# Optimization experiments

Hardware: AMD Instinct MI355X
Metric: run time of the kernel (lower is better)

The kernel has to match this reference:

```python
import jax, jax.numpy as jnp
import numpy as np

KS = 2            # kernel_size
NUM_SHARED = 3    # len(num_shared_channels)
NBR_PARAM = 3     # nbr_param_layers
COUT = 128        # num_shared_channels[-1] == num_inputs
NUM_INPUTS = 128
D_R = 320         # ts2vec_output_dims
GEN_LEN = NBR_PARAM * COUT * COUT * KS


def _causal_conv(x, w, b, d):
    # x: [N, Ci, T], w: [Co, Ci, K], b: [Co]; left-pad (K-1)*d == pad+chomp in torch
    N, Ci, T = x.shape
    K = w.shape[-1]
    pad = (K - 1) * d
    xp = jnp.pad(x, ((0, 0), (0, 0), (pad, 0)))
    out = jnp.zeros((N, w.shape[0], T), dtype=x.dtype)
    for k in range(K):  # K==2, tiny static loop
        out = out + jnp.einsum('oc,nct->not', w[:, :, k], xp[:, :, k * d:k * d + T])
    return out + b[None, :, None]


def _causal_conv_group(x, w, d):
    # groups=N conv with per-sample weights. x: [N, C, T], w: [N, Co, C, K], no bias
    N, C, T = x.shape
    K = w.shape[-1]
    pad = (K - 1) * d
    xp = jnp.pad(x, ((0, 0), (0, 0), (pad, 0)))
    out = jnp.zeros((N, w.shape[1], T), dtype=x.dtype)
    for k in range(K):
        out = out + jnp.einsum('noc,nct->not', w[..., k], xp[:, :, k * d:k * d + T])
    return out


def setup_inputs() -> dict:
    key = jax.random.key(0)
    ks = jax.random.split(key, 12)
    N, T = 16, 1024
    x = jax.random.normal(ks[0], (N, T, NUM_INPUTS), dtype=jnp.float32)
    r = jax.random.normal(ks[1], (N, D_R), dtype=jnp.float32)
    # shared TemporalBlock params (in==out==COUT, so no downsample conv)
    wscale = 1.0 / np.sqrt(COUT * KS)
    shared_w1 = wscale * jax.random.normal(ks[2], (NUM_SHARED, COUT, COUT, KS), dtype=jnp.float32)
    shared_b1 = 0.01 * jax.random.normal(ks[3], (NUM_SHARED, COUT), dtype=jnp.float32)
    shared_w2 = wscale * jax.random.normal(ks[4], (NUM_SHARED, COUT, COUT, KS), dtype=jnp.float32)
    shared_b2 = 0.01 * jax.random.normal(ks[5], (NUM_SHARED, COUT), dtype=jnp.float32)
    # hypernetwork (f_param_generator) + additive base weights (last_conv_layers)
    fparam_W = 0.01 * jax.random.normal(ks[6], (GEN_LEN, D_R), dtype=jnp.float32)
    fparam_b = 0.01 * jax.random.normal(ks[7], (GEN_LEN,), dtype=jnp.float32)
    last_bias = 0.001 * jax.random.normal(ks[8], (GEN_LEN,), dtype=jnp.float32) + 1.0 / (KS * COUT)
    # output head
    lin_W = (1.0 / np.sqrt(COUT)) * jax.random.normal(ks[9], (NUM_INPUTS, COUT), dtype=jnp.float32)
    lin_b = 0.01 * jax.random.normal(ks[10], (NUM_INPUTS,), dtype=jnp.float32)
    return {"x": x, "r": r, "f_out_same_in_size": 1,
            "shared_w1": shared_w1, "shared_b1": shared_b1,
            "shared_w2": shared_w2, "shared_b2": shared_b2,
            "fparam_W": fparam_W, "fparam_b": fparam_b, "last_bias": last_bias,
            "lin_W": lin_W, "lin_b": lin_b}


def reference(x, r, f_out_same_in_size, shared_w1, shared_b1, shared_w2, shared_b2,
              fparam_W, fparam_b, last_bias, lin_W, lin_b):
    N, T, _ = x.shape
    h = jnp.swapaxes(x, 1, 2)  # [N, C, T]
    # shared TemporalBlocks (dropout p=0 -> identity)
    for i in range(NUM_SHARED):
        d = 2 ** i
        res = h
        a = jax.nn.relu(_causal_conv(h, shared_w1[i], shared_b1[i], d))
        a = jax.nn.relu(_causal_conv(a, shared_w2[i], shared_b2[i], d))
        h = jax.nn.relu(a + res)
    # hypernet-generated per-sample grouped conv layers
    gen = r @ fparam_W.T + fparam_b + last_bias           # [N, GEN_LEN]
    allw = gen.reshape(NBR_PARAM, N, COUT, COUT, KS)      # same layout as torch .view
    for i in range(NBR_PARAM):
        d = 2 ** (NUM_SHARED + i)
        res = h
        c = _causal_conv_group(h, allw[i], d)
        h = jax.nn.relu(jax.nn.relu(c) + res)             # relu(dropout(relu(c)) + res), p=0
    out = jnp.einsum('nct,oc->nto', h, lin_W) + lin_b     # [N, T, NUM_INPUTS]
    if not f_out_same_in_size:
        out = out[:, -1, :]
    return out
```

## Files before the change

### kernel.cpp

```cpp
#include <hip/hip_runtime.h>

#define NB    16
#define TLEN  1024
#define CCH   128
#define DR    320

typedef _Float16 h8 __attribute__((ext_vector_type(8)));
typedef _Float16 h4 __attribute__((ext_vector_type(4)));
typedef _Float16 h2 __attribute__((ext_vector_type(2)));
typedef float    f4 __attribute__((ext_vector_type(4)));

__device__ __forceinline__ void gload16h(const _Float16* g, _Float16* l) {
  __builtin_amdgcn_global_load_lds(
      (const __attribute__((address_space(1))) void*)g,
      (__attribute__((address_space(3))) void*)l, 16, 0, 0);
}
__device__ __forceinline__ void gload16f(const float* g, float* l) {
  __builtin_amdgcn_global_load_lds(
      (const __attribute__((address_space(1))) void*)g,
      (__attribute__((address_space(3))) void*)l, 16, 0, 0);
}

__global__ __launch_bounds__(256) void k_init(const float* __restrict__ x,
                                              const float* __restrict__ w1,
                                              const float* __restrict__ w2,
                                              const float* __restrict__ linw,
                                              const float* __restrict__ fb,
                                              const float* __restrict__ lb,
                                              _Float16* __restrict__ h0,
                                              _Float16* __restrict__ Wsh,
                                              _Float16* __restrict__ linWh,
                                              float* __restrict__ fblb2) {
  int i = blockIdx.x * 256 + threadIdx.x;
  const float4* src = (const float4*)x + (size_t)i * 2;
  float4 a = src[0], b = src[1];
  h8 v;
  v[0] = (_Float16)a.x; v[1] = (_Float16)a.y; v[2] = (_Float16)a.z; v[3] = (_Float16)a.w;
  v[4] = (_Float16)b.x; v[5] = (_Float16)b.y; v[6] = (_Float16)b.z; v[7] = (_Float16)b.w;
  *(h8*)(h0 + (size_t)i * 8) = v;

  if (i < 6 * 32768) {
    int c = i & 127, k = (i >> 7) & 1, o = (i >> 8) & 127, i3 = i >> 15;
    const float* srcw = (i3 < 3) ? (w1 + i3 * 32768) : (w2 + (i3 - 3) * 32768);
    Wsh[i] = (_Float16)srcw[(o * 128 + c) * 2 + k];
  }
  if (i < 16384) linWh[i] = (_Float16)linw[i];
  if (i < 98304) fblb2[i] = fb[i] + lb[i];
}

struct SGen {
  float buf[3][32 * DR];
  float csc[4][16][16];
  float fbl[512];
};
struct SPair {
  _Float16 hin[84 * 128];
  _Float16 a[80 * 128];
};
union alignas(16) SU { SGen g; SPair p; };

__device__ __forceinline__ void gen_body(SGen& S, int bid, int tid,
                                         const float* __restrict__ r,
                                         const float* __restrict__ fW,
                                         const float* __restrict__ fblb2,
                                         _Float16* __restrict__ wg) {
  constexpr int NT = 16;
  const size_t rbase = (size_t)bid * 512;

  const int l = tid & 63, w = tid >> 6;
  const int l15 = l & 15, lh = l >> 4;
  const int rt = w >> 1, kh = w & 1;

  f4 rx[5], ry[5];
  const float* rp = r + l15 * DR + kh * 160 + lh * 8;
#pragma unroll
  for (int cb = 0; cb < 5; cb++) {
    rx[cb] = *(const f4*)(rp + cb * 32);
    ry[cb] = *(const f4*)(rp + cb * 32 + 4);
  }
  if (tid < 128) gload16f(fblb2 + rbase + tid * 4, S.fbl + tid * 4);
#pragma unroll
  for (int t = 0; t < 3; t++) {
    const float* s = fW + (rbase + (size_t)t * 32) * DR;
#pragma unroll
    for (int i = 0; i < 10; i++) {
      int f = tid + i * 256;
      gload16f(s + (size_t)f * 4, (float*)S.buf[t] + (size_t)f * 4);
    }
  }
  h8 bfr[5];
#pragma unroll
  for (int cb = 0; cb < 5; cb++) {
    h8 v;
    v[0] = (_Float16)rx[cb][0]; v[1] = (_Float16)rx[cb][1];
    v[2] = (_Float16)rx[cb][2]; v[3] = (_Float16)rx[cb][3];
    v[4] = (_Float16)ry[cb][0]; v[5] = (_Float16)ry[cb][1];
    v[6] = (_Float16)ry[cb][2]; v[7] = (_Float16)ry[cb][3];
    bfr[cb] = v;
  }
  asm volatile("s_waitcnt vmcnt(20) lgkmcnt(0)" ::: "memory");
  __builtin_amdgcn_s_barrier();
  __builtin_amdgcn_sched_barrier(0);

  const int rn = tid >> 4, rk = (tid >> 3) & 1, rcq = tid & 7;

  for (int j = 0; j < NT; j++) {
    const float* bp = (const float*)S.buf[j % 3];
    f4 acc = {0.f, 0.f, 0.f, 0.f};
    const float* arow = bp + (rt * 16 + l15) * DR + kh * 160 + lh * 8;
#pragma unroll
    for (int cb = 0; cb < 5; cb++) {
      f4 x = *(const f4*)(arow + cb * 32);
      f4 y = *(const f4*)(arow + cb * 32 + 4);
      h8 a;
      a[0] = (_Float16)x[0]; a[1] = (_Float16)x[1];
      a[2] = (_Float16)x[2]; a[3] = (_Float16)x[3];
      a[4] = (_Float16)y[0]; a[5] = (_Float16)y[1];
      a[6] = (_Float16)y[2]; a[7] = (_Float16)y[3];
      acc = __builtin_amdgcn_mfma_f32_16x16x32_f16(a, bfr[cb], acc, 0, 0, 0);
    }
#pragma unroll
    for (int rr = 0; rr < 4; rr++) S.csc[w][lh * 4 + rr][l15] = acc[rr];

    asm volatile("s_waitcnt lgkmcnt(0)" ::: "memory");
    __builtin_amdgcn_s_barrier();
    __builtin_amdgcn_sched_barrier(0);

    {
      const unsigned g32 = (unsigned)(rbase + (size_t)j * 32);
      const unsigned G = g32 >> 15, o = (g32 >> 8) & 127u, c0 = (g32 & 255u) >> 1;
      h2 v2;
#pragma unroll
      for (int i = 0; i < 2; i++) {
        int rl32 = (rcq * 2 + i) * 2 + rk;
        int hp = (rl32 >> 4) * 2, rr2 = rl32 & 15;
        float s = S.csc[hp][rr2][rn] + S.csc[hp + 1][rr2][rn] + S.fbl[j * 32 + rl32];
        v2[i] = (_Float16)s;
      }
      unsigned q = 3u * (unsigned)rn + G;
      *(h2*)&wg[(((size_t)q * 128 + o) * 2 + rk) * 128 + c0 + rcq * 2] = v2;
    }
    __builtin_amdgcn_sched_barrier(0);

    if (j + 3 < NT) {
      float* dstb = (float*)S.buf[j % 3];
      const float* src = fW + (rbase + (size_t)(j + 3) * 32) * DR;
#pragma unroll
      for (int i = 0; i < 10; i++) {
        int f = tid + i * 256;
        gload16f(src + (size_t)f * 4, dstb + (size_t)f * 4);
      }
    }

    if (j + 4 <= NT)
      asm volatile("s_waitcnt vmcnt(22) lgkmcnt(0)" ::: "memory");
    else if (j + 3 == NT)
      asm volatile("s_waitcnt vmcnt(12) lgkmcnt(0)" ::: "memory");
    else
      asm volatile("s_waitcnt vmcnt(0) lgkmcnt(0)" ::: "memory");
    __builtin_amdgcn_s_barrier();
    __builtin_amdgcn_sched_barrier(0);
  }
}

template <int D>
__device__ __forceinline__ void pair_body(SPair& S, int tx, int n, int tid,
                                          const _Float16* in, _Float16* out,
                                          const _Float16* w1p, const _Float16* w2p,
                                          const float* b1p, const float* b2p) {
  constexpr int HA = 16;
  constexpr int HI = HA + D;
  constexpr int RIN = 80 + D;
  static_assert(RIN * 128 <= sizeof(SPair::hin) / sizeof(_Float16), "hin size");
  _Float16* hin_l = S.hin;
  _Float16* a_l = S.a;
  const int t0 = tx * 64;
  const _Float16* inN = in + (size_t)n * (TLEN * CCH);

  if (tx == 0) {
    for (int f = tid; f < HI * 16; f += 256)
      *(int4*)(hin_l + (size_t)f * 8) = make_int4(0, 0, 0, 0);
    for (int f = HI * 16 + tid; f < RIN * 16; f += 256) {
      int p = f >> 4, l16 = f & 15;
      int c8 = (l16 ^ (p & 15)) << 3;
      gload16h(inN + (t0 - HI + p) * 128 + c8, hin_l + f * 8);
    }
  } else {
    for (int f = tid; f < RIN * 16; f += 256) {
      int p = f >> 4, l16 = f & 15;
      int c8 = (l16 ^ (p & 15)) << 3;
      gload16h(inN + (t0 - HI + p) * 128 + c8, hin_l + f * 8);
    }
  }
  __syncthreads();

  const int l = tid & 63, w = tid >> 6;
  const int l15 = l & 15, lh = l >> 4;
  const int o0 = w * 32;

  f4 acc1[2][5] = {};
#pragma unroll
  for (int tap = 0; tap < 2; tap++) {
#pragma unroll
    for (int cb = 0; cb < 4; cb++) {
      const int c0 = cb * 32 + lh * 8;
      h8 a[2], bfr[5];
#pragma unroll
      for (int i2 = 0; i2 < 2; i2++) {
        int o = o0 + i2 * 16 + l15;
        a[i2] = *(const h8*)&w1p[(o * 2 + tap) * 128 + c0];
      }
#pragma unroll
      for (int jt = 0; jt < 5; jt++) {
        int p = jt * 16 + l15 + tap * D;
        int cs = c0 ^ ((p & 15) << 3);
        bfr[jt] = *(const h8*)&hin_l[p * 128 + cs];
      }
#pragma unroll
      for (int i2 = 0; i2 < 2; i2++)
#pragma unroll
        for (int jt = 0; jt < 5; jt++)
          acc1[i2][jt] = __builtin_amdgcn_mfma_f32_16x16x32_f16(
              a[i2], bfr[jt], acc1[i2][jt], 0, 0, 0);
    }
  }
#pragma unroll
  for (int i2 = 0; i2 < 2; i2++) {
    f4 bv = *(const f4*)&b1p[o0 + i2 * 16 + lh * 4];
    const int base8 = o0 + i2 * 16 + (lh >> 1) * 8;
    const int sub = (lh & 1) * 4;
#pragma unroll
    for (int jt = 0; jt < 5; jt++) {
      int p = jt * 16 + l15;
      h4 sv;
      if (tx == 0 && jt == 0) {
        sv[0] = sv[1] = sv[2] = sv[3] = (_Float16)0.f;
      } else {
        f4 v = acc1[i2][jt];
#pragma unroll
        for (int rr = 0; rr < 4; rr++) sv[rr] = (_Float16)fmaxf(v[rr] + bv[rr], 0.f);
      }
      *(h4*)&a_l[p * 128 + (base8 ^ ((p & 15) << 3)) + sub] = sv;
    }
  }
  __syncthreads();

  f4 acc2[2][4] = {};
#pragma unroll
  for (int tap = 0; tap < 2; tap++) {
#pragma unroll
    for (int cb = 0; cb < 4; cb++) {
      const int c0 = cb * 32 + lh * 8;
      h8 a[2], bfr[4];
#pragma unroll
      for (int i2 = 0; i2 < 2; i2++) {
        int o = o0 + i2 * 16 + l15;
        a[i2] = *(const h8*)&w2p[(o * 2 + tap) * 128 + c0];
      }
#pragma unroll
      for (int jt = 0; jt < 4; jt++) {
        int pa = jt * 16 + l15 + (HA - D) + tap * D;
        int cs = c0 ^ ((pa & 15) << 3);
        bfr[jt] = *(const h8*)&a_l[pa * 128 + cs];
      }
#pragma unroll
      for (int i2 = 0; i2 < 2; i2++)
#pragma unroll
        for (int jt = 0; jt < 4; jt++)
          acc2[i2][jt] = __builtin_amdgcn_mfma_f32_16x16x32_f16(
              a[i2], bfr[jt], acc2[i2][jt], 0, 0, 0);
    }
  }

  _Float16* outN = out + (size_t)n * (TLEN * CCH);
#pragma unroll
  for (int i2 = 0; i2 < 2; i2++) {
    f4 bv = *(const f4*)&b2p[o0 + i2 * 16 + lh * 4];
    const int base8 = o0 + i2 * 16 + (lh >> 1) * 8;
    const int sub = (lh & 1) * 4;
#pragma unroll
    for (int jt = 0; jt < 4; jt++) {
      int t = t0 + jt * 16 + l15;
      int pr = jt * 16 + l15 + HA + D;
      h4 rv = *(const h4*)&hin_l[pr * 128 + (base8 ^ ((pr & 15) << 3)) + sub];
      f4 v = acc2[i2][jt];
      h4 sv;
#pragma unroll
      for (int rr = 0; rr < 4; rr++) {
        float z = fmaxf(v[rr] + bv[rr], 0.f);
        sv[rr] = (_Float16)fmaxf(z + (float)rv[rr], 0.f);
      }
      *(h4*)&outN[t * 128 + o0 + i2 * 16 + lh * 4] = sv;
    }
  }
}

__global__ __launch_bounds__(256, 1) void k_genpair(
    const float* __restrict__ r, const float* __restrict__ fW,
    const float* __restrict__ fblb2, _Float16* __restrict__ wg,
    const _Float16* __restrict__ h0, _Float16* __restrict__ h1,
    const _Float16* __restrict__ Wsh,
    const float* __restrict__ b1, const float* __restrict__ b2) {
  __shared__ SU su;
  const int bid = blockIdx.x, tid = threadIdx.x;
  if (bid < 192) {
    gen_body(su.g, bid, tid, r, fW, fblb2, wg);
  } else {
    int q = bid - 192;
    pair_body<1>(su.p, q & 15, q >> 4, tid, h0, h1,
                 Wsh, Wsh + 3 * 32768, b1, b2);
  }
}

template <int D, int NJ, bool GOUT>
__device__ __forceinline__ void pstage(const _Float16* __restrict__ w1p,
                                       const _Float16* __restrict__ w2p,
                                       const float* __restrict__ b1p,
                                       const float* __restrict__ b2p,
                                       const _Float16* __restrict__ inb,
                                       _Float16* __restrict__ ab,
                                       _Float16* __restrict__ outb,
                                       _Float16* __restrict__ goutN, int t0,
                                       int zlimA, int zlimO, int tid) {
  constexpr int NA = NJ + 1;
  const int l = tid & 63, w = tid >> 6;
  const int l15 = l & 15, lh = l >> 4;
  const int o0 = w * 32;
  const int base8 = o0 + (lh >> 1) * 8;
  const int sub = (lh & 1) * 4;

  f4 acc1[2][NA] = {};
#pragma unroll
  for (int tap = 0; tap < 2; tap++) {
#pragma unroll
    for (int cb = 0; cb < 4; cb++) {
      const int c0 = cb * 32 + lh * 8;
      h8 a[2], bfr[NA];
#pragma unroll
      for (int i2 = 0; i2 < 2; i2++) {
        int o = o0 + i2 * 16 + l15;
        a[i2] = *(const h8*)&w1p[(o * 2 + tap) * 128 + c0];
      }
#pragma unroll
      for (int jt = 0; jt < NA; jt++) {
        int p = jt * 16 + l15 + tap * D;
        int cs = c0 ^ ((p & 15) << 3);
        bfr[jt] = *(const h8*)&inb[p * 128 + cs];
      }
#pragma unroll
      for (int i2 = 0; i2 < 2; i2++)
#pragma unroll
        for (int jt = 0; jt < NA; jt++)
          acc1[i2][jt] = __builtin_amdgcn_mfma_f32_16x16x32_f16(
              a[i2], bfr[jt], acc1[i2][jt], 0, 0, 0);
    }
  }
#pragma unroll
  for (int i2 = 0; i2 < 2; i2++) {
    f4 bv = *(const f4*)&b1p[o0 + i2 * 16 + lh * 4];
    const int b8 = base8 + i2 * 16;
#pragma unroll
    for (int jt = 0; jt < NA; jt++) {
      int q = jt * 16 + l15;
      h4 sv;
      if (q < zlimA) {
        sv[0] = sv[1] = sv[2] = sv[3] = (_Float16)0.f;
      } else {
        f4 v = acc1[i2][jt];
#pragma unroll
        for (int rr = 0; rr < 4; rr++) sv[rr] = (_Float16)fmaxf(v[rr] + bv[rr], 0.f);
      }
      *(h4*)&ab[q * 128 + (b8 ^ ((q & 15) << 3)) + sub] = sv;
    }
  }
  __syncthreads();

  f4 acc2[2][NJ] = {};
#pragma unroll
  for (int tap = 0; tap < 2; tap++) {
#pragma unroll
    for (int cb = 0; cb < 4; cb++) {
      const int c0 = cb * 32 + lh * 8;
      h8 a[2], bfr[NJ];
#pragma unroll
      for (int i2 = 0; i2 < 2; i2++) {
        int o = o0 + i2 * 16 + l15;
        a[i2] = *(const h8*)&w2p[(o * 2 + tap) * 128 + c0];
      }
#pragma unroll
      for (int jt = 0; jt < NJ; jt++) {
        int pa = jt * 16 + l15 + (16 - 2 * D) + tap * D;
        int cs = c0 ^ ((pa & 15) << 3);
        bfr[jt] = *(const h8*)&ab[pa * 128 + cs];
      }
#pragma unroll
      for (int i2 = 0; i2 < 2; i2++)
#pragma unroll
        for (int jt = 0; jt < NJ; jt++)
          acc2[i2][jt] = __builtin_amdgcn_mfma_f32_16x16x32_f16(
              a[i2], bfr[jt], acc2[i2][jt], 0, 0, 0);
    }
  }
#pragma unroll
  for (int i2 = 0; i2 < 2; i2++) {
    f4 bv = *(const f4*)&b2p[o0 + i2 * 16 + lh * 4];
    const int b8 = base8 + i2 * 16;
#pragma unroll
    for (int jt = 0; jt < NJ; jt++) {
      int r = jt * 16 + l15;
      int pr = r + 16;
      h4 sv;
      if (r < zlimO) {
        sv[0] = sv[1] = sv[2] = sv[3] = (_Float16)0.f;
      } else {
        h4 rv = *(const h4*)&inb[pr * 128 + (b8 ^ ((pr & 15) << 3)) + sub];
        f4 v = acc2[i2][jt];
#pragma unroll
        for (int rr = 0; rr < 4; rr++) {
          float z = fmaxf(v[rr] + bv[rr], 0.f);
          sv[rr] = (_Float16)fmaxf(z + (float)rv[rr], 0.f);
        }
      }
      if (GOUT) {
        int t = t0 + r;
        *(h4*)&goutN[t * 128 + o0 + i2 * 16 + lh * 4] = sv;
      } else {
        *(h4*)&outb[r * 128 + (b8 ^ (l15 << 3)) + sub] = sv;
      }
    }
  }
}

__global__ __launch_bounds__(256) void k_pair24(const _Float16* __restrict__ in,
                                                _Float16* __restrict__ out,
                                                const _Float16* __restrict__ Wsh,
                                                const float* __restrict__ b1,
                                                const float* __restrict__ b2) {
  __shared__ _Float16 B0[104 * 128];
  __shared__ _Float16 B1[96 * 128];
  __shared__ _Float16 B2[88 * 128];
  const int tid = threadIdx.x;
  const int tx = blockIdx.x, n = blockIdx.y;
  const int t0 = tx * 64;
  const _Float16* inN = in + (size_t)n * (TLEN * CCH);

  for (int f = 96 * 16 + tid; f < 104 * 16; f += 256)
    *(int4*)(B0 + (size_t)f * 8) = make_int4(0, 0, 0, 0);
  for (int f = 80 * 16 + tid; f < 88 * 16; f += 256)
    *(int4*)(B2 + (size_t)f * 8) = make_int4(0, 0, 0, 0);

  if (tx == 0) {
    for (int f = tid; f < 32 * 16; f += 256)
      *(int4*)(B0 + (size_t)f * 8) = make_int4(0, 0, 0, 0);
    for (int f = 32 * 16 + tid; f < 96 * 16; f += 256) {
      int p = f >> 4, l16 = f & 15;
      int c8 = (l16 ^ (p & 15)) << 3;
      gload16h(inN + (t0 - 32 + p) * 128 + c8, B0 + f * 8);
    }
  } else {
    for (int f = tid; f < 96 * 16; f += 256) {
      int p = f >> 4, l16 = f & 15;
      int c8 = (l16 ^ (p & 15)) << 3;
      gload16h(inN + (t0 - 32 + p) * 128 + c8, B0 + f * 8);
    }
  }
  __syncthreads();

  pstage<2, 5, false>(Wsh + 1 * 32768, Wsh + 4 * 32768, b1 + 128, b2 + 128,
                      B0, B1, B2, nullptr, t0,
                      (tx == 0) ? 30 : 0, (tx == 0) ? 16 : 0, tid);
  __syncthreads();
  pstage<4, 4, true>(Wsh + 2 * 32768, Wsh + 5 * 32768, b1 + 256, b2 + 256,
                     B2, B1, nullptr,
                     out + (size_t)n * (TLEN * CCH), t0,
                     (tx == 0) ? 12 : 0, 0, tid);
}

template <int D, int NJ>
__device__ __forceinline__ void gstage(const _Float16* __restrict__ Wl,
                                       const _Float16* __restrict__ inb,
                                       _Float16* __restrict__ outb,
                                       int zlim, int tid) {
  const int l = tid & 63, w = tid >> 6;
  const int l15 = l & 15, lh = l >> 4;
  const int o0 = w * 32;
  f4 acc[2][NJ] = {};

#pragma unroll
  for (int tap = 0; tap < 2; tap++) {
#pragma unroll
    for (int cb = 0; cb < 4; cb++) {
      const int c0 = cb * 32 + 8 * lh;
      h8 a[2], bfr[NJ];
#pragma unroll
      for (int i2 = 0; i2 < 2; i2++) {
        int o = o0 + i2 * 16 + l15;
        int cs = c0 ^ ((o & 15) << 3);
        a[i2] = *(const h8*)&Wl[(o * 2 + tap) * 128 + cs];
      }
#pragma unroll
      for (int jt = 0; jt < NJ; jt++) {
        int p = jt * 16 + l15 + tap * D;
        int cs = c0 ^ ((p & 15) << 3);
        bfr[jt] = *(const h8*)&inb[p * 128 + cs];
      }
#pragma unroll
      for (int i2 = 0; i2 < 2; i2++)
#pragma unroll
        for (int jt = 0; jt < NJ; jt++)
          acc[i2][jt] = __builtin_amdgcn_mfma_f32_16x16x32_f16(
              a[i2], bfr[jt], acc[i2][jt], 0, 0, 0);
    }
  }

#pragma unroll
  for (int i2 = 0; i2 < 2; i2++) {
    const int base8 = o0 + i2 * 16 + (lh >> 1) * 8;
    const int sub = (lh & 1) * 4;
#pragma unroll
    for (int jt = 0; jt < NJ; jt++) {
      int rrow = jt * 16 + l15;
      int pr = rrow + D;
      h4 sv;
      if (rrow < zlim) {
        sv[0] = sv[1] = sv[2] = sv[3] = (_Float16)0.f;
      } else {
        h4 rv = *(const h4*)&inb[pr * 128 + (base8 ^ ((pr & 15) << 3)) + sub];
        f4 v = acc[i2][jt];
#pragma unroll
        for (int rr = 0; rr < 4; rr++) {
          float z = fmaxf(v[rr], 0.f);
          sv[rr] = (_Float16)fmaxf(z + (float)rv[rr], 0.f);
        }
      }
      *(h4*)&outb[rrow * 128 + (base8 ^ (l15 << 3)) + sub] = sv;
    }
  }
}

__global__ __launch_bounds__(256, 1) void k_group(const _Float16* __restrict__ in,
                                                  float* __restrict__ outp,
                                                  const _Float16* __restrict__ wg,
                                                  const _Float16* __restrict__ linWh,
                                                  const float* __restrict__ lbias) {
  __shared__ _Float16 bufA[120 * 128];
  __shared__ _Float16 bufB[112 * 128];
  __shared__ _Float16 Wl[256 * 128];
  const int tid = threadIdx.x;
  const int bid = blockIdx.x;
  const int n = (bid & 7) | (((bid >> 3) & 1) << 3);
  const int tx = bid >> 4;
  const int t0 = tx * 64;
  const _Float16* inN = in + (size_t)n * (TLEN * CCH);
  const _Float16* wp1 = wg + (size_t)n * 32768;
  const _Float16* wp2 = wg + 524288 + (size_t)n * 32768;
  const _Float16* wp3 = wg + 1048576 + (size_t)n * 32768;

  if (tx == 0) {
    for (int f = tid; f < 56 * 16; f += 256)
      *(int4*)(bufA + (size_t)f * 8) = make_int4(0, 0, 0, 0);
    for (int f = 56 * 16 + tid; f < 120 * 16; f += 256) {
      int p = f >> 4, l16 = f & 15;
      int c8 = (l16 ^ (p & 15)) << 3;
      gload16h(inN + (t0 - 56 + p) * 128 + c8, bufA + f * 8);
    }
  } else {
    for (int f = tid; f < 120 * 16; f += 256) {
      int p = f >> 4, l16 = f & 15;
      int c8 = (l16 ^ (p & 15)) << 3;
      gload16h(inN + (t0 - 56 + p) * 128 + c8, bufA + f * 8);
    }
  }
  for (int f = tid; f < 4096; f += 256) {
    int row = f >> 4, l16 = f & 15;
    int c8 = (l16 ^ ((row >> 1) & 15)) << 3;
    gload16h(wp1 + row * 128 + c8, Wl + f * 8);
  }
  __syncthreads();

  gstage<8, 7>(Wl, bufA, bufB, (tx == 0) ? 48 : 0, tid);
  __syncthreads();
  for (int f = tid; f < 4096; f += 256) {
    int row = f >> 4, l16 = f & 15;
    int c8 = (l16 ^ ((row >> 1) & 15)) << 3;
    gload16h(wp2 + row * 128 + c8, Wl + f * 8);
  }
  __syncthreads();

  gstage<16, 6>(Wl, bufB, bufA, (tx == 0) ? 32 : 0, tid);
  __syncthreads();
  for (int f = tid; f < 4096; f += 256) {
    int row = f >> 4, l16 = f & 15;
    int c8 = (l16 ^ ((row >> 1) & 15)) << 3;
    gload16h(wp3 + row * 128 + c8, Wl + f * 8);
  }
  __syncthreads();

  gstage<32, 4>(Wl, bufA, bufB, 0, tid);
  __syncthreads();

  const int l = tid & 63, w = tid >> 6;
  const int l15 = l & 15, lh = l >> 4;
  const int o0 = w * 32;
  f4 acc3[2][4] = {};
#pragma unroll
  for (int cb = 0; cb < 4; cb++) {
    const int c0 = cb * 32 + lh * 8;
    h8 a[2], bfr[4];
#pragma unroll
    for (int i2 = 0; i2 < 2; i2++) {
      int o = o0 + i2 * 16 + l15;
      a[i2] = *(const h8*)&linWh[o * 128 + c0];
    }
#pragma unroll
    for (int jt = 0; jt < 4; jt++) {
      int p = jt * 16 + l15;
      int cs = c0 ^ ((p & 15) << 3);
      bfr[jt] = *(const h8*)&bufB[p * 128 + cs];
    }
#pragma unroll
    for (int i2 = 0; i2 < 2; i2++)
#pragma unroll
      for (int jt = 0; jt < 4; jt++)
        acc3[i2][jt] = __builtin_amdgcn_mfma_f32_16x16x32_f16(
            a[i2], bfr[jt], acc3[i2][jt], 0, 0, 0);
  }

#pragma unroll
  for (int i2 = 0; i2 < 2; i2++) {
    int o = o0 + i2 * 16 + lh * 4;
    f4 bv = *(const f4*)&lbias[o];
#pragma unroll
    for (int jt = 0; jt < 4; jt++) {
      int t = t0 + jt * 16 + l15;
      f4 v = acc3[i2][jt];
      float4 sv = make_float4(v[0] + bv[0], v[1] + bv[1], v[2] + bv[2], v[3] + bv[3]);
      *(float4*)&outp[((size_t)n * TLEN + t) * CCH + o] = sv;
    }
  }
}

extern "C" void kernel_launch(void* const* d_in, const int* in_sizes, int n_in,
                              void* d_out, int out_size, void* d_ws, size_t ws_size,
                              hipStream_t stream) {
  const float* x  = (const float*)d_in[0];
  const float* r  = (const float*)d_in[1];
  const float* w1 = (const float*)d_in[3];
  const float* b1 = (const float*)d_in[4];
  const float* w2 = (const float*)d_in[5];
  const float* b2 = (const float*)d_in[6];
  const float* fW = (const float*)d_in[7];
  const float* fb = (const float*)d_in[8];
  const float* lb = (const float*)d_in[9];
  const float* lw = (const float*)d_in[10];
  const float* lbias = (const float*)d_in[11];
  float* out = (float*)d_out;

  _Float16* h0    = (_Float16*)d_ws;
  _Float16* h1    = h0 + 2097152;
  _Float16* Wsh   = h1 + 2097152;
  _Float16* linWh = Wsh + 393216;
  _Float16* Wg    = linWh + 16384;
  float*    fblb2 = (float*)(Wg + 1572864);

  k_init<<<1024, 256, 0, stream>>>(x, w1, w2, lw, fb, lb, h0, Wsh, linWh, fblb2);
  k_genpair<<<448, 256, 0, stream>>>(r, fW, fblb2, Wg, h0, h1, Wsh, b1, b2);
  k_pair24<<<dim3(16, 16), 256, 0, stream>>>(h1, h0, Wsh, b1, b2);
  k_group<<<256, 256, 0, stream>>>(h0, out, Wg, linWh, lbias);
}
```

Measured before the change: 68.91 us.

## Fuse input fp16 conversion and bias sum into the gen/pair kernel

The init kernel no longer converts x to fp16 into a workspace buffer or precomputes fb+lb. The first pair stage now reads fp32 x directly, converts it in registers and writes it to LDS, and the generator blocks load fb and lb separately and add them at use. This removes an 8 MB fp32 read plus a 4 MB fp16 write-then-reread and shrinks the init grid. The cost is that the pair loads are now synchronous register loads instead of async global-to-LDS loads, and each gen block does one extra small LDS load.

```diff
diff --git a/kernel.cpp b/kernel.cpp
--- a/kernel.cpp
+++ b/kernel.cpp
@@ -21,37 +21,25 @@
       (__attribute__((address_space(3))) void*)l, 16, 0, 0);
 }
 
-__global__ __launch_bounds__(256) void k_init(const float* __restrict__ x,
-                                              const float* __restrict__ w1,
+__global__ __launch_bounds__(256) void k_init(const float* __restrict__ w1,
                                               const float* __restrict__ w2,
                                               const float* __restrict__ linw,
-                                              const float* __restrict__ fb,
-                                              const float* __restrict__ lb,
-                                              _Float16* __restrict__ h0,
                                               _Float16* __restrict__ Wsh,
-                                              _Float16* __restrict__ linWh,
-                                              float* __restrict__ fblb2) {
+                                              _Float16* __restrict__ linWh) {
   int i = blockIdx.x * 256 + threadIdx.x;
-  const float4* src = (const float4*)x + (size_t)i * 2;
-  float4 a = src[0], b = src[1];
-  h8 v;
-  v[0] = (_Float16)a.x; v[1] = (_Float16)a.y; v[2] = (_Float16)a.z; v[3] = (_Float16)a.w;
-  v[4] = (_Float16)b.x; v[5] = (_Float16)b.y; v[6] = (_Float16)b.z; v[7] = (_Float16)b.w;
-  *(h8*)(h0 + (size_t)i * 8) = v;
-
-  if (i < 6 * 32768) {
+  {
     int c = i & 127, k = (i >> 7) & 1, o = (i >> 8) & 127, i3 = i >> 15;
     const float* srcw = (i3 < 3) ? (w1 + i3 * 32768) : (w2 + (i3 - 3) * 32768);
     Wsh[i] = (_Float16)srcw[(o * 128 + c) * 2 + k];
   }
   if (i < 16384) linWh[i] = (_Float16)linw[i];
-  if (i < 98304) fblb2[i] = fb[i] + lb[i];
 }
 
 struct SGen {
   float buf[3][32 * DR];
   float csc[4][16][16];
   float fbl[512];
+  float lbl[512];
 };
 struct SPair {
   _Float16 hin[84 * 128];
@@ -62,7 +50,8 @@
 __device__ __forceinline__ void gen_body(SGen& S, int bid, int tid,
                                          const float* __restrict__ r,
                                          const float* __restrict__ fW,
-                                         const float* __restrict__ fblb2,
+                                         const float* __restrict__ fb,
+                                         const float* __restrict__ lb,
                                          _Float16* __restrict__ wg) {
   constexpr int NT = 16;
   const size_t rbase = (size_t)bid * 512;
@@ -78,7 +67,10 @@
     rx[cb] = *(const f4*)(rp + cb * 32);
     ry[cb] = *(const f4*)(rp + cb * 32 + 4);
   }
-  if (tid < 128) gload16f(fblb2 + rbase + tid * 4, S.fbl + tid * 4);
+  if (tid < 128) {
+    gload16f(fb + rbase + tid * 4, S.fbl + tid * 4);
+    gload16f(lb + rbase + tid * 4, S.lbl + tid * 4);
+  }
 #pragma unroll
   for (int t = 0; t < 3; t++) {
     const float* s = fW + (rbase + (size_t)t * 32) * DR;
@@ -134,7 +126,8 @@
       for (int i = 0; i < 2; i++) {
         int rl32 = (rcq * 2 + i) * 2 + rk;
         int hp = (rl32 >> 4) * 2, rr2 = rl32 & 15;
-        float s = S.csc[hp][rr2][rn] + S.csc[hp + 1][rr2][rn] + S.fbl[j * 32 + rl32];
+        float s = S.csc[hp][rr2][rn] + S.csc[hp + 1][rr2][rn] +
+                  S.fbl[j * 32 + rl32] + S.lbl[j * 32 + rl32];
         v2[i] = (_Float16)s;
       }
       unsigned q = 3u * (unsigned)rn + G;
@@ -165,7 +158,7 @@
 
 template <int D>
 __device__ __forceinline__ void pair_body(SPair& S, int tx, int n, int tid,
-                                          const _Float16* in, _Float16* out,
+                                          const float* xin, _Float16* out,
                                           const _Float16* w1p, const _Float16* w2p,
                                           const float* b1p, const float* b2p) {
   constexpr int HA = 16;
@@ -175,22 +168,24 @@
   _Float16* hin_l = S.hin;
   _Float16* a_l = S.a;
   const int t0 = tx * 64;
-  const _Float16* inN = in + (size_t)n * (TLEN * CCH);
-
+  const float* xN = xin + (size_t)n * (TLEN * CCH);
+
+  const int flo = (tx == 0) ? HI * 16 : 0;
   if (tx == 0) {
     for (int f = tid; f < HI * 16; f += 256)
       *(int4*)(hin_l + (size_t)f * 8) = make_int4(0, 0, 0, 0);
-    for (int f = HI * 16 + tid; f < RIN * 16; f += 256) {
-      int p = f >> 4, l16 = f & 15;
-      int c8 = (l16 ^ (p & 15)) << 3;
-      gload16h(inN + (t0 - HI + p) * 128 + c8, hin_l + f * 8);
-    }
-  } else {
-    for (int f = tid; f < RIN * 16; f += 256) {
-      int p = f >> 4, l16 = f & 15;
-      int c8 = (l16 ^ (p & 15)) << 3;
-      gload16h(inN + (t0 - HI + p) * 128 + c8, hin_l + f * 8);
-    }
+  }
+  for (int f = flo + tid; f < RIN * 16; f += 256) {
+    int p = f >> 4, l16 = f & 15;
+    int c8 = (l16 ^ (p & 15)) << 3;
+    const float* sp = xN + (size_t)(t0 - HI + p) * 128 + c8;
+    f4 xa = *(const f4*)sp, xb = *(const f4*)(sp + 4);
+    h8 v;
+    v[0] = (_Float16)xa[0]; v[1] = (_Float16)xa[1];
+    v[2] = (_Float16)xa[2]; v[3] = (_Float16)xa[3];
+    v[4] = (_Float16)xb[0]; v[5] = (_Float16)xb[1];
+    v[6] = (_Float16)xb[2]; v[7] = (_Float16)xb[3];
+    *(h8*)(hin_l + (size_t)f * 8) = v;
   }
   __syncthreads();
 
@@ -297,17 +292,18 @@
 
 __global__ __launch_bounds__(256, 1) void k_genpair(
     const float* __restrict__ r, const float* __restrict__ fW,
-    const float* __restrict__ fblb2, _Float16* __restrict__ wg,
-    const _Float16* __restrict__ h0, _Float16* __restrict__ h1,
+    const float* __restrict__ fb, const float* __restrict__ lb,
+    _Float16* __restrict__ wg,
+    const float* __restrict__ x, _Float16* __restrict__ h1,
     const _Float16* __restrict__ Wsh,
     const float* __restrict__ b1, const float* __restrict__ b2) {
   __shared__ SU su;
   const int bid = blockIdx.x, tid = threadIdx.x;
   if (bid < 192) {
-    gen_body(su.g, bid, tid, r, fW, fblb2, wg);
+    gen_body(su.g, bid, tid, r, fW, fb, lb, wg);
   } else {
     int q = bid - 192;
-    pair_body<1>(su.p, q & 15, q >> 4, tid, h0, h1,
+    pair_body<1>(su.p, q & 15, q >> 4, tid, x, h1,
                  Wsh, Wsh + 3 * 32768, b1, b2);
   }
 }
@@ -661,10 +657,9 @@
   _Float16* Wsh   = h1 + 2097152;
   _Float16* linWh = Wsh + 393216;
   _Float16* Wg    = linWh + 16384;
-  float*    fblb2 = (float*)(Wg + 1572864);
-
-  k_init<<<1024, 256, 0, stream>>>(x, w1, w2, lw, fb, lb, h0, Wsh, linWh, fblb2);
-  k_genpair<<<448, 256, 0, stream>>>(r, fW, fblb2, Wg, h0, h1, Wsh, b1, b2);
+
+  k_init<<<768, 256, 0, stream>>>(w1, w2, lw, Wsh, linWh);
+  k_genpair<<<448, 256, 0, stream>>>(r, fW, fb, lb, Wg, x, h1, Wsh, b1, b2);
   k_pair24<<<dim3(16, 16), 256, 0, stream>>>(h1, h0, Wsh, b1, b2);
   k_group<<<256, 256, 0, stream>>>(h0, out, Wg, linWh, lbias);
 }
```

Measured after the change: 69.38 us. Within noise of the previous version (+0.7%).
